# Kernel tuning notes

Measured on AMD Instinct MI355X. Metric: run time of the kernel, lower is better.

Reference implementation:

```python
import jax, jax.numpy as jnp
import numpy as np

N_EMBED = 16384
EMBED_DIM = 256
BETA = 1.0  # default forward arg


def setup_inputs() -> dict:
    key = jax.random.key(0)
    k1, k2 = jax.random.split(key)
    z = jax.random.normal(k1, (8, EMBED_DIM, 32, 32), dtype=jnp.float32)
    # nn.Embedding init: uniform(-1/n_embed, 1/n_embed)
    embed_w = jax.random.uniform(k2, (N_EMBED, EMBED_DIM), dtype=jnp.float32,
                                 minval=-1.0 / N_EMBED, maxval=1.0 / N_EMBED)
    return {"z": z, "embed_w": embed_w}


def reference(z, embed_w):
    B, C, H, W = z.shape
    zb = jnp.transpose(z, (0, 2, 3, 1))            # (B,H,W,C)
    zf = zb.reshape(B * H * W, C)                  # (BHW, C)
    # squared L2 distances to every code: ||z||^2 + ||e||^2 - 2 z.e
    d = (jnp.sum(zf ** 2, axis=1, keepdims=True)
         + jnp.sum(embed_w ** 2, axis=1)
         - 2.0 * jnp.einsum('bd,nd->bn', zf, embed_w))  # (BHW, n_embed)
    idx = jnp.argmin(d, axis=1)                    # (BHW,)
    z_q = embed_w[idx].reshape(B, H, W, C)         # codebook gather
    loss = (BETA * jnp.mean((jax.lax.stop_gradient(z_q) - zb) ** 2)
            + jnp.mean((z_q - jax.lax.stop_gradient(zb)) ** 2))
    # straight-through estimator
    z_q = zb + jax.lax.stop_gradient(z_q - zb)
    z_q = jnp.transpose(z_q, (0, 3, 1, 2))         # (B,C,H,W)
    return z_q, loss
```

## Files before the change

kernel.cpp:

```cpp
#include <hip/hip_runtime.h>
#include <hip/hip_bf16.h>
#include <stdint.h>


typedef __attribute__((ext_vector_type(8))) short bf16x8;
typedef __attribute__((ext_vector_type(8))) unsigned short ushort8v;
typedef __attribute__((ext_vector_type(4))) float f32x4;

__device__ __forceinline__ unsigned short f2bf(float f) {
  unsigned u = __float_as_uint(f);
  return (unsigned short)((u + 0x7FFFu + ((u >> 16) & 1u)) >> 16);
}

typedef const __attribute__((address_space(1))) unsigned char* gas1;
typedef __attribute__((address_space(3))) unsigned char* las3;
__device__ __forceinline__ void cp16g(const void* g, void* l) {
  __builtin_amdgcn_global_load_lds((gas1)g, (las3)l, 16, 0, 0);
}

__global__ void k_prep(const float* __restrict__ z, const float* __restrict__ ew,
                       unsigned short* __restrict__ zp, unsigned short* __restrict__ ep,
                       float* __restrict__ h2, float* __restrict__ out) {
  __shared__ float tile[32][132];
  int bid = blockIdx.x;
  int t = threadIdx.x;
  if (bid < 512) {
    int b = bid >> 6, ct = (bid >> 3) & 7, hwt = bid & 7;
    const float* src = z + b * 262144 + ct * 32768 + hwt * 128;
#pragma unroll
    for (int it = 0; it < 4; ++it) {
      int cell = it * 1024 + t * 4;
      int cl = cell >> 7, hl = cell & 127;
      float4 v = *(const float4*)(src + cl * 1024 + hl);
      *(float4*)(&tile[cl][hl]) = v;
    }
    __syncthreads();
    int mt = b * 8 + hwt;
    unsigned short* dst = zp + mt * 32768 + ct * 4096;
#pragma unroll
    for (int it = 0; it < 2; ++it) {
      int cell = it * 256 + t;
      int kg = cell >> 7, r = cell & 127;
      ushort8v v;
#pragma unroll
      for (int j = 0; j < 8; ++j) v[j] = f2bf(tile[kg * 8 + j][r]);
      *(ushort8v*)(dst + cell * 8) = v;
    }
  } else {
    if (bid == 512 && t == 0) out[2097152] = 0.0f;
    int n = (bid - 512) * 32 + (t >> 3);
    int nb = n >> 7, col = n & 127;
    float s = 0.0f;
#pragma unroll
    for (int it = 0; it < 4; ++it) {
      int cellk = (t & 7) + it * 8;
      const float4 x = *(const float4*)(ew + n * 256 + cellk * 8);
      const float4 y = *(const float4*)(ew + n * 256 + cellk * 8 + 4);
      s += x.x * x.x + x.y * x.y + x.z * x.z + x.w * x.w
         + y.x * y.x + y.y * y.y + y.z * y.z + y.w * y.w;
      int ks = cellk >> 2, kg = cellk & 3;
      ushort8v v;
      v[0] = f2bf(x.x); v[1] = f2bf(x.y); v[2] = f2bf(x.z); v[3] = f2bf(x.w);
      v[4] = f2bf(y.x); v[5] = f2bf(y.y); v[6] = f2bf(y.z); v[7] = f2bf(y.w);
      *(ushort8v*)(ep + nb * 32768 + ks * 4096 + kg * 1024 + col * 8) = v;
    }
#pragma unroll
    for (int off = 1; off <= 4; off <<= 1) s += __shfl_xor(s, off);
    if ((t & 7) == 0) h2[n] = -0.5f * s;
  }
}

__global__ __launch_bounds__(256, 2) void k_main(
    const unsigned short* __restrict__ zp, const unsigned short* __restrict__ ep,
    const float* __restrict__ h2, int2* __restrict__ partial) {
  __shared__ unsigned char ring[4][16384];
  __shared__ float hbuf[1024];
  int seg = blockIdx.x;
  int mt = blockIdx.y;
  int t = threadIdx.x, wv = t >> 6, lane = t & 63;
  int l15 = lane & 15, kg = lane >> 4;

  bf16x8 av[16];
  const unsigned short* abase = zp + mt * 32768;
#pragma unroll
  for (int m = 0; m < 2; ++m)
#pragma unroll
    for (int ks = 0; ks < 8; ++ks)
      av[m * 8 + ks] = *(const bf16x8*)(abase + ks * 4096 + kg * 1024 +
                                        (wv * 32 + m * 16 + l15) * 8);

  const unsigned char* bsrc = (const unsigned char*)ep + seg * 524288;
  const unsigned char* bstage = bsrc + wv * 1024 + lane * 16;
  int ldsw = wv * 1024;

  cp16g((const unsigned char*)(h2 + seg * 1024) + ldsw + lane * 16,
        (unsigned char*)hbuf + ldsw);
#pragma unroll
  for (int i = 0; i < 4; ++i)
    cp16g(bstage + i * 4096, &ring[0][i * 4096 + ldsw]);
  __builtin_amdgcn_sched_barrier(0);
#pragma unroll
  for (int i = 0; i < 4; ++i)
    cp16g(bstage + 16384 + i * 4096, &ring[1][i * 4096 + ldsw]);

  f32x4 acc[2][8];
  float best[2][4];
#pragma unroll
  for (int m = 0; m < 2; ++m)
#pragma unroll
    for (int r = 0; r < 4; ++r) best[m][r] = -3.4e38f;

#define KSTEP(PH, NB, DOSTAGE, VM)                                              \
  {                                                                             \
    asm volatile("s_waitcnt vmcnt(" VM ")" ::: "memory");                       \
    __builtin_amdgcn_s_barrier();                                               \
    if (DOSTAGE) {                                                              \
      const unsigned char* sg = bstage + ((NB) * 4 + (PH) + 2) * 16384;         \
      _Pragma("unroll") for (int i = 0; i < 4; ++i)                             \
        cp16g(sg + i * 4096, &ring[((PH) + 2) & 3][i * 4096 + ldsw]);           \
    }                                                                           \
    if ((PH) == 0) {                                                            \
      _Pragma("unroll") for (int nf = 0; nf < 8; ++nf) {                        \
        float h = hbuf[(NB) * 128 + nf * 16 + l15];                             \
        acc[0][nf] = (f32x4){h, h, h, h};                                       \
        acc[1][nf] = acc[0][nf];                                                \
      }                                                                         \
    }                                                                           \
    __builtin_amdgcn_s_setprio(1);                                              \
    _Pragma("unroll") for (int k2 = 0; k2 < 2; ++k2) {                          \
      bf16x8 bv[8];                                                             \
      _Pragma("unroll") for (int nf = 0; nf < 8; ++nf)                          \
        bv[nf] = *(const bf16x8*)(&ring[(PH)][k2 * 8192 + kg * 2048 +           \
                                             (nf * 16 + l15) * 16]);            \
      _Pragma("unroll") for (int m = 0; m < 2; ++m)                             \
        _Pragma("unroll") for (int nf = 0; nf < 8; ++nf)                        \
          acc[m][nf] = __builtin_amdgcn_mfma_f32_16x16x32_bf16(                 \
              av[m * 8 + (PH) * 2 + k2], bv[nf], acc[m][nf], 0, 0, 0);          \
    }                                                                           \
    __builtin_amdgcn_s_setprio(0);                                              \
    if ((PH) == 3) {                                                            \
      unsigned colbase = (unsigned)((NB) * 128 + l15);                          \
      _Pragma("unroll") for (int m = 0; m < 2; ++m)                             \
        _Pragma("unroll") for (int nf = 0; nf < 8; ++nf) {                      \
          unsigned lcol = colbase + nf * 16u;                                   \
          _Pragma("unroll") for (int r = 0; r < 4; ++r) {                       \
            unsigned p = (__float_as_uint(acc[m][nf][r]) & 0xFFFFF800u) | lcol; \
            best[m][r] = fmaxf(best[m][r], __uint_as_float(p));                 \
          }                                                                     \
        }                                                                       \
    }                                                                           \
  }

#pragma unroll 1
  for (int nb = 0; nb < 7; ++nb) {
    KSTEP(0, nb, 1, "4")
    KSTEP(1, nb, 1, "4")
    KSTEP(2, nb, 1, "4")
    KSTEP(3, nb, 1, "4")
  }
  KSTEP(0, 7, 1, "4")
  KSTEP(1, 7, 1, "4")
  KSTEP(2, 7, 0, "4")
  KSTEP(3, 7, 0, "0")
#undef KSTEP

#pragma unroll
  for (int m = 0; m < 2; ++m)
#pragma unroll
    for (int r = 0; r < 4; ++r) {
      float bvv = best[m][r];
#pragma unroll
      for (int off = 1; off <= 8; off <<= 1) bvv = fmaxf(bvv, __shfl_xor(bvv, off));
      if (l15 == 0) {
        unsigned bits = __float_as_uint(bvv);
        int gidx = seg * 1024 + (int)(bits & 0x7FFu);
        int row = mt * 128 + wv * 32 + m * 16 + kg * 4 + r;
        partial[seg * 8192 + row] = make_int2((int)bits, gidx);
      }
    }
}

__global__ void k_fin(const int2* __restrict__ partial, const float* __restrict__ ew,
                      const float* __restrict__ z, float* __restrict__ out) {
  __shared__ float tile[32][260];
  __shared__ int codeIdx[32];
  int bid = blockIdx.x;
  int b = bid >> 5, pxt = bid & 31;
  int t = threadIdx.x, wv = t >> 6, lane = t & 63;
  if (t < 32) {
    int row = b * 1024 + pxt * 32 + t;
    float bb = -3.4e38f;
    int bi = 0;
#pragma unroll
    for (int s = 0; s < 16; ++s) {
      int2 p = partial[s * 8192 + row];
      float v = __int_as_float(p.x);
      if (v > bb) { bb = v; bi = p.y; }
    }
    codeIdx[t] = bi;
  }
  __syncthreads();
#pragma unroll
  for (int i = 0; i < 8; ++i) {
    int px = wv * 8 + i;
    int idx = codeIdx[px];
    float4 v = *(const float4*)(ew + idx * 256 + lane * 4);
    *(float4*)(&tile[px][lane * 4]) = v;
  }
  __syncthreads();
  float ls = 0.0f;
  int zbase = b * 262144 + pxt * 32;
#pragma unroll
  for (int j = 0; j < 8; ++j) {
    int c = wv * 64 + j * 8 + (lane >> 3);
    int p4 = (lane & 7) * 4;
    float4 q;
    q.x = tile[p4][c]; q.y = tile[p4 + 1][c]; q.z = tile[p4 + 2][c]; q.w = tile[p4 + 3][c];
    const float* zp_ = z + zbase + c * 1024 + p4;
    float4 zv = *(const float4*)zp_;
    float dx = q.x - zv.x, dy = q.y - zv.y, dz = q.z - zv.z, dw = q.w - zv.w;
    ls += dx * dx + dy * dy + dz * dz + dw * dw;
    *(float4*)(out + zbase + c * 1024 + p4) = q;
  }
#pragma unroll
  for (int off = 32; off; off >>= 1) ls += __shfl_xor(ls, off);
  if (lane == 0) atomicAdd(out + 2097152, ls * (2.0f / 2097152.0f));
}

extern "C" void kernel_launch(void* const* d_in, const int* in_sizes, int n_in,
                              void* d_out, int out_size, void* d_ws, size_t ws_size,
                              hipStream_t stream) {
  const float* z = (const float*)d_in[0];
  const float* ew = (const float*)d_in[1];
  float* out = (float*)d_out;
  unsigned char* ws = (unsigned char*)d_ws;
  unsigned short* zp = (unsigned short*)ws;
  unsigned short* ep = (unsigned short*)(ws + (4u << 20));
  float* h2 = (float*)(ws + (12u << 20));
  int2* partial = (int2*)(ws + (12u << 20) + 65536);

  k_prep<<<1024, 256, 0, stream>>>(z, ew, zp, ep, h2, out);
  k_main<<<dim3(16, 64), 256, 0, stream>>>(zp, ep, h2, partial);
  k_fin<<<256, 256, 0, stream>>>(partial, ew, z, out);
}
```

Measured before the change: 152.3 us.

## Shrink LDS ring to three stages for three blocks per CU and coalesce codebook prep

The main kernel's shared-memory ring drops from four 16KB stages to three, tracked by rotating read/write offsets, and launch bounds rise to allow three blocks per CU. The per-code norm bias is now added during the argmin epilogue instead of being used to seed the accumulators. The prep kernel stages codebook rows through shared memory so that both global reads and the packed bf16 writes are coalesced. In exchange, prefetch depth is shorter (two stages ahead with three buffers, so reads and writes may race unless the barriers order them), register pressure rises under the tighter launch bound, and the rotating offsets add scalar work.

```diff
diff --git a/kernel.cpp b/kernel.cpp
--- a/kernel.cpp
+++ b/kernel.cpp
@@ -21,10 +21,11 @@
 __global__ void k_prep(const float* __restrict__ z, const float* __restrict__ ew,
                        unsigned short* __restrict__ zp, unsigned short* __restrict__ ep,
                        float* __restrict__ h2, float* __restrict__ out) {
-  __shared__ float tile[32][132];
+  __shared__ unsigned char smem[16896];
   int bid = blockIdx.x;
   int t = threadIdx.x;
   if (bid < 512) {
+    float (*tile)[132] = (float (*)[132])smem;
     int b = bid >> 6, ct = (bid >> 3) & 7, hwt = bid & 7;
     const float* src = z + b * 262144 + ct * 32768 + hwt * 128;
 #pragma unroll
@@ -47,33 +48,43 @@
       *(ushort8v*)(dst + cell * 8) = v;
     }
   } else {
+    unsigned short (*et)[264] = (unsigned short (*)[264])smem;
     if (bid == 512 && t == 0) out[2097152] = 0.0f;
-    int n = (bid - 512) * 32 + (t >> 3);
-    int nb = n >> 7, col = n & 127;
-    float s = 0.0f;
+    int n0 = (bid - 512) * 32;
+    int lane = t & 63;
 #pragma unroll
     for (int it = 0; it < 4; ++it) {
-      int cellk = (t & 7) + it * 8;
-      const float4 x = *(const float4*)(ew + n * 256 + cellk * 8);
-      const float4 y = *(const float4*)(ew + n * 256 + cellk * 8 + 4);
-      s += x.x * x.x + x.y * x.y + x.z * x.z + x.w * x.w
-         + y.x * y.x + y.y * y.y + y.z * y.z + y.w * y.w;
-      int ks = cellk >> 2, kg = cellk & 3;
+      int c = it * 8 + (t >> 5);
+      int k0 = (t & 31) * 8;
+      const float4 x = *(const float4*)(ew + (n0 + c) * 256 + k0);
+      const float4 y = *(const float4*)(ew + (n0 + c) * 256 + k0 + 4);
+      float s = x.x * x.x + x.y * x.y + x.z * x.z + x.w * x.w
+              + y.x * y.x + y.y * y.y + y.z * y.z + y.w * y.w;
       ushort8v v;
       v[0] = f2bf(x.x); v[1] = f2bf(x.y); v[2] = f2bf(x.z); v[3] = f2bf(x.w);
       v[4] = f2bf(y.x); v[5] = f2bf(y.y); v[6] = f2bf(y.z); v[7] = f2bf(y.w);
-      *(ushort8v*)(ep + nb * 32768 + ks * 4096 + kg * 1024 + col * 8) = v;
-    }
-#pragma unroll
-    for (int off = 1; off <= 4; off <<= 1) s += __shfl_xor(s, off);
-    if ((t & 7) == 0) h2[n] = -0.5f * s;
-  }
-}
-
-__global__ __launch_bounds__(256, 2) void k_main(
+      *(ushort8v*)(&et[c][k0]) = v;
+#pragma unroll
+      for (int off = 1; off <= 16; off <<= 1) s += __shfl_xor(s, off);
+      if ((lane & 31) == 0) h2[n0 + c] = -0.5f * s;
+    }
+    __syncthreads();
+    int nb = n0 >> 7, col0 = n0 & 127;
+#pragma unroll
+    for (int it = 0; it < 4; ++it) {
+      int cellk = it * 8 + (t >> 5);
+      int c = t & 31;
+      int ks = cellk >> 2, kg = cellk & 3;
+      ushort8v v = *(const ushort8v*)(&et[c][cellk * 8]);
+      *(ushort8v*)(ep + nb * 32768 + ks * 4096 + kg * 1024 + (col0 + c) * 8) = v;
+    }
+  }
+}
+
+__global__ __launch_bounds__(256, 3) void k_main(
     const unsigned short* __restrict__ zp, const unsigned short* __restrict__ ep,
     const float* __restrict__ h2, int2* __restrict__ partial) {
-  __shared__ unsigned char ring[4][16384];
+  __shared__ unsigned char ring[49152];
   __shared__ float hbuf[1024];
   int seg = blockIdx.x;
   int mt = blockIdx.y;
@@ -97,11 +108,11 @@
         (unsigned char*)hbuf + ldsw);
 #pragma unroll
   for (int i = 0; i < 4; ++i)
-    cp16g(bstage + i * 4096, &ring[0][i * 4096 + ldsw]);
+    cp16g(bstage + i * 4096, &ring[i * 4096 + ldsw]);
   __builtin_amdgcn_sched_barrier(0);
 #pragma unroll
   for (int i = 0; i < 4; ++i)
-    cp16g(bstage + 16384 + i * 4096, &ring[1][i * 4096 + ldsw]);
+    cp16g(bstage + 16384 + i * 4096, &ring[16384 + i * 4096 + ldsw]);
 
   f32x4 acc[2][8];
   float best[2][4];
@@ -109,6 +120,8 @@
   for (int m = 0; m < 2; ++m)
 #pragma unroll
     for (int r = 0; r < 4; ++r) best[m][r] = -3.4e38f;
+
+  unsigned rd = 0u, wr = 32768u;
 
 #define KSTEP(PH, NB, DOSTAGE, VM)                                              \
   {                                                                             \
@@ -117,21 +130,18 @@
     if (DOSTAGE) {                                                              \
       const unsigned char* sg = bstage + ((NB) * 4 + (PH) + 2) * 16384;         \
       _Pragma("unroll") for (int i = 0; i < 4; ++i)                             \
-        cp16g(sg + i * 4096, &ring[((PH) + 2) & 3][i * 4096 + ldsw]);           \
+        cp16g(sg + i * 4096, &ring[wr + i * 4096 + ldsw]);                      \
     }                                                                           \
     if ((PH) == 0) {                                                            \
-      _Pragma("unroll") for (int nf = 0; nf < 8; ++nf) {                        \
-        float h = hbuf[(NB) * 128 + nf * 16 + l15];                             \
-        acc[0][nf] = (f32x4){h, h, h, h};                                       \
-        acc[1][nf] = acc[0][nf];                                                \
-      }                                                                         \
+      _Pragma("unroll") for (int nf = 0; nf < 8; ++nf)                          \
+        acc[0][nf] = acc[1][nf] = (f32x4){0.f, 0.f, 0.f, 0.f};                  \
     }                                                                           \
     __builtin_amdgcn_s_setprio(1);                                              \
     _Pragma("unroll") for (int k2 = 0; k2 < 2; ++k2) {                          \
       bf16x8 bv[8];                                                             \
       _Pragma("unroll") for (int nf = 0; nf < 8; ++nf)                          \
-        bv[nf] = *(const bf16x8*)(&ring[(PH)][k2 * 8192 + kg * 2048 +           \
-                                             (nf * 16 + l15) * 16]);            \
+        bv[nf] = *(const bf16x8*)(&ring[rd + k2 * 8192 + kg * 2048 +            \
+                                        (nf * 16 + l15) * 16]);                 \
       _Pragma("unroll") for (int m = 0; m < 2; ++m)                             \
         _Pragma("unroll") for (int nf = 0; nf < 8; ++nf)                        \
           acc[m][nf] = __builtin_amdgcn_mfma_f32_16x16x32_bf16(                 \
@@ -140,15 +150,18 @@
     __builtin_amdgcn_s_setprio(0);                                              \
     if ((PH) == 3) {                                                            \
       unsigned colbase = (unsigned)((NB) * 128 + l15);                          \
-      _Pragma("unroll") for (int m = 0; m < 2; ++m)                             \
-        _Pragma("unroll") for (int nf = 0; nf < 8; ++nf) {                      \
-          unsigned lcol = colbase + nf * 16u;                                   \
+      _Pragma("unroll") for (int nf = 0; nf < 8; ++nf) {                        \
+        float h = hbuf[(NB) * 128 + nf * 16 + l15];                             \
+        unsigned lcol = colbase + nf * 16u;                                     \
+        _Pragma("unroll") for (int m = 0; m < 2; ++m)                           \
           _Pragma("unroll") for (int r = 0; r < 4; ++r) {                       \
-            unsigned p = (__float_as_uint(acc[m][nf][r]) & 0xFFFFF800u) | lcol; \
+            unsigned p = (__float_as_uint(acc[m][nf][r] + h) & 0xFFFFF800u) | lcol; \
             best[m][r] = fmaxf(best[m][r], __uint_as_float(p));                 \
           }                                                                     \
-        }                                                                       \
-    }                                                                           \
+      }                                                                         \
+    }                                                                           \
+    rd = (rd == 32768u) ? 0u : rd + 16384u;                                     \
+    wr = (wr == 32768u) ? 0u : wr + 16384u;                                     \
   }
 
 #pragma unroll 1
```

New measurement: 188.1 us. +23.5%, slower.
